# Optimization experiments

Measured on AMD Instinct MI355X. Metric: run time of the kernel, lower is better.

## Reference

```python
import jax, jax.numpy as jnp
import numpy as np


def setup_inputs() -> dict:
    key = jax.random.key(0)
    k1, k2, k3, k4 = jax.random.split(key, 4)
    N, F, E, M = 50000, 128, 1600000, 1024
    return {
        "molec_feature_vectures": jax.random.normal(k1, (N, F), dtype=jnp.float32),
        "W": jax.random.normal(k2, (F, F), dtype=jnp.float32),
        "mo_neighbour_indices": jax.random.randint(k3, (2, E), 0, N, dtype=jnp.int64),
        "mo_mol_id": jax.random.randint(k4, (E,), 0, M, dtype=jnp.int64),
        "n_output": M,
    }


def reference(molec_feature_vectures, W, mo_neighbour_indices, mo_mol_id, n_output):
    # Gather endpoint features for each neighbor pair: [E, F]
    fi = molec_feature_vectures[mo_neighbour_indices[0]]
    fj = molec_feature_vectures[mo_neighbour_indices[1]]
    # Symmetric bilinear form (mode='pes'): s_n = fi_n . (W + W^T) . fj_n
    Ws = W + W.T  # [F, F]
    # Fuse as (fi @ Ws) * fj summed over F to avoid a 3-operand einsum blowup
    scalars = jnp.einsum('ni,ij,nj->n', fi, Ws, fj)  # [E]
    # Segment-sum per molecule
    res = jax.ops.segment_sum(scalars, mo_mol_id, num_segments=n_output)  # [M]
    return res
```

## Files before the change

kernel.cpp:

```cpp
#include <hip/hip_runtime.h>
#include <hip/hip_bf16.h>

#define FDIM 128
#define BROWS 32
#define NBLK 256
#define NSLICE 32

typedef __attribute__((ext_vector_type(8))) short short8v;
typedef __attribute__((ext_vector_type(4))) float f32x4;

static __device__ __forceinline__ unsigned short f2bf(float x) {
    unsigned u = __float_as_uint(x);
    unsigned r = 0x7fffu + ((u >> 16) & 1u);
    return (unsigned short)((u + r) >> 16);
}
static __device__ __forceinline__ float bf2f(unsigned short h) {
    return __uint_as_float((unsigned)h << 16);
}
static __device__ __forceinline__ float bf_lo(unsigned u) { return __uint_as_float(u << 16); }
static __device__ __forceinline__ float bf_hi(unsigned u) { return __uint_as_float(u & 0xffff0000u); }

static __device__ __forceinline__ void split2(float v, short& h, short& l) {
    unsigned short hh = f2bf(v);
    h = (short)hh;
    l = (short)f2bf(v - bf2f(hh));
}

__global__ __launch_bounds__(512, 4) void gemm_mfma(
    const float* __restrict__ Fm, const float* __restrict__ W,
    unsigned short* __restrict__ Gbf, int N) {
    __shared__ unsigned short sH[128 * 136];
    __shared__ unsigned short sL[128 * 136];

    for (int idx = threadIdx.x; idx < 128 * 128; idx += 512) {
        int i = idx >> 7, j = idx & 127;
        float w = W[idx] + W[j * 128 + i];
        short h, l;
        split2(w, h, l);
        sH[i * 136 + j] = (unsigned short)h;
        sL[i * 136 + j] = (unsigned short)l;
    }
    __syncthreads();

    const int wid  = threadIdx.x >> 6;
    const int lane = threadIdx.x & 63;
    const int ar   = lane & 15;
    const int kg   = lane >> 4;
    const int row0 = blockIdx.x * 128 + wid * 16;
    const int gr   = row0 + ar;
    const bool rv  = gr < N;
    const float* fp = Fm + (size_t)gr * FDIM;

    f32x4 acc[8];
#pragma unroll
    for (int t = 0; t < 8; ++t) acc[t] = (f32x4){0.f, 0.f, 0.f, 0.f};

#pragma unroll
    for (int ks = 0; ks < 4; ++ks) {
        const int k0 = ks * 32 + kg * 8;
        float4 fa = make_float4(0.f, 0.f, 0.f, 0.f);
        float4 fb = make_float4(0.f, 0.f, 0.f, 0.f);
        if (rv) {
            fa = *(const float4*)(fp + k0);
            fb = *(const float4*)(fp + k0 + 4);
        }
        short8v ah, al;
        {
            short h, l;
            split2(fa.x, h, l); ah[0] = h; al[0] = l;
            split2(fa.y, h, l); ah[1] = h; al[1] = l;
            split2(fa.z, h, l); ah[2] = h; al[2] = l;
            split2(fa.w, h, l); ah[3] = h; al[3] = l;
            split2(fb.x, h, l); ah[4] = h; al[4] = l;
            split2(fb.y, h, l); ah[5] = h; al[5] = l;
            split2(fb.z, h, l); ah[6] = h; al[6] = l;
            split2(fb.w, h, l); ah[7] = h; al[7] = l;
        }
#pragma unroll
        for (int ct = 0; ct < 8; ++ct) {
            const short8v bh = *(const short8v*)(sH + (ct * 16 + ar) * 136 + k0);
            const short8v bl = *(const short8v*)(sL + (ct * 16 + ar) * 136 + k0);
            acc[ct] = __builtin_amdgcn_mfma_f32_16x16x32_bf16(ah, bh, acc[ct], 0, 0, 0);
            acc[ct] = __builtin_amdgcn_mfma_f32_16x16x32_bf16(ah, bl, acc[ct], 0, 0, 0);
            acc[ct] = __builtin_amdgcn_mfma_f32_16x16x32_bf16(al, bh, acc[ct], 0, 0, 0);
        }
    }

#pragma unroll
    for (int r = 0; r < 4; ++r) {
        const int orow = row0 + kg * 4 + r;
        if (orow < N) {
#pragma unroll
            for (int ct = 0; ct < 8; ++ct)
                Gbf[(size_t)orow * FDIM + ct * 16 + ar] = f2bf(acc[ct][r]);
        }
    }
}

__global__ __launch_bounds__(256) void k_hist(const int* __restrict__ idx, int E,
                                              int nb, unsigned* __restrict__ M) {
    extern __shared__ unsigned cnt[];
    for (int i = threadIdx.x; i < nb; i += 256) cnt[i] = 0;
    __syncthreads();
    int chunk = (E + NBLK - 1) / NBLK;
    int s = blockIdx.x * chunk;
    int e_end = min(E, s + chunk);
    for (int e = s + threadIdx.x; e < e_end; e += 256) {
        int i1 = idx[E + e];
        atomicAdd(&cnt[i1 >> 5], 1u);
    }
    __syncthreads();
    for (int i = threadIdx.x; i < nb; i += 256)
        M[(size_t)blockIdx.x * nb + i] = cnt[i];
}

__global__ __launch_bounds__(256) void k_mscan2(unsigned* __restrict__ M, int nb,
                                                unsigned* __restrict__ tot) {
    int b = blockIdx.x * 4 + (threadIdx.x >> 6);
    int lane = threadIdx.x & 63;
    if (b >= nb) return;
    unsigned m0 = M[(size_t)(4 * lane + 0) * nb + b];
    unsigned m1 = M[(size_t)(4 * lane + 1) * nb + b];
    unsigned m2 = M[(size_t)(4 * lane + 2) * nb + b];
    unsigned m3 = M[(size_t)(4 * lane + 3) * nb + b];
    unsigned s = m0 + m1 + m2 + m3;
    unsigned incl = s;
#pragma unroll
    for (int d = 1; d < 64; d <<= 1) {
        unsigned u = __shfl_up(incl, d, 64);
        if (lane >= d) incl += u;
    }
    unsigned run = incl - s;
    M[(size_t)(4 * lane + 0) * nb + b] = run; run += m0;
    M[(size_t)(4 * lane + 1) * nb + b] = run; run += m1;
    M[(size_t)(4 * lane + 2) * nb + b] = run; run += m2;
    M[(size_t)(4 * lane + 3) * nb + b] = run;
    if (lane == 63) tot[b] = incl;
}

__global__ __launch_bounds__(256) void k_bscan(const unsigned* __restrict__ tot, int nb,
                                               unsigned* __restrict__ bucketStart) {
    __shared__ unsigned wS[4];
    int t = threadIdx.x;
    unsigned v0, v1, v2, v3, v4, v5, v6, v7;
    int b0 = t * 8;
    v0 = (b0 + 0 < nb) ? tot[b0 + 0] : 0u;
    v1 = (b0 + 1 < nb) ? tot[b0 + 1] : 0u;
    v2 = (b0 + 2 < nb) ? tot[b0 + 2] : 0u;
    v3 = (b0 + 3 < nb) ? tot[b0 + 3] : 0u;
    v4 = (b0 + 4 < nb) ? tot[b0 + 4] : 0u;
    v5 = (b0 + 5 < nb) ? tot[b0 + 5] : 0u;
    v6 = (b0 + 6 < nb) ? tot[b0 + 6] : 0u;
    v7 = (b0 + 7 < nb) ? tot[b0 + 7] : 0u;
    unsigned l0 = 0, l1 = v0, l2 = l1 + v1, l3 = l2 + v2, l4 = l3 + v3,
             l5 = l4 + v4, l6 = l5 + v5, l7 = l6 + v6;
    unsigned s = l7 + v7;
    int lane = t & 63, wid = t >> 6;
    unsigned incl = s;
    for (int d = 1; d < 64; d <<= 1) {
        unsigned u = __shfl_up(incl, d, 64);
        if (lane >= d) incl += u;
    }
    if (lane == 63) wS[wid] = incl;
    __syncthreads();
    unsigned wOff = 0;
    for (int i = 0; i < wid; ++i) wOff += wS[i];
    unsigned base = wOff + incl - s;
    if (b0 + 0 < nb) bucketStart[b0 + 0] = base + l0;
    if (b0 + 1 < nb) bucketStart[b0 + 1] = base + l1;
    if (b0 + 2 < nb) bucketStart[b0 + 2] = base + l2;
    if (b0 + 3 < nb) bucketStart[b0 + 3] = base + l3;
    if (b0 + 4 < nb) bucketStart[b0 + 4] = base + l4;
    if (b0 + 5 < nb) bucketStart[b0 + 5] = base + l5;
    if (b0 + 6 < nb) bucketStart[b0 + 6] = base + l6;
    if (b0 + 7 < nb) bucketStart[b0 + 7] = base + l7;
    if (t == 255) bucketStart[nb] = base + s;
}

__global__ __launch_bounds__(256) void k_scatter(const int* __restrict__ idx,
                                                 const int* __restrict__ mol, int E,
                                                 int nb, const unsigned* __restrict__ M,
                                                 const unsigned* __restrict__ bucketStart,
                                                 unsigned* __restrict__ sortedE) {
    extern __shared__ unsigned cur[];
    for (int i = threadIdx.x; i < nb; i += 256)
        cur[i] = M[(size_t)blockIdx.x * nb + i] + bucketStart[i];
    __syncthreads();
    int chunk = (E + NBLK - 1) / NBLK;
    int s = blockIdx.x * chunk;
    int e_end = min(E, s + chunk);
    for (int e = s + threadIdx.x; e < e_end; e += 256) {
        int i0 = idx[e];
        int i1 = idx[E + e];
        int m  = mol[e];
        int b  = i1 >> 5;
        int loc = i1 & 31;
        unsigned pos = atomicAdd(&cur[b], 1u);
        sortedE[pos] = (unsigned)i0 | ((unsigned)m << 16) | ((unsigned)loc << 26);
    }
}

__global__ __launch_bounds__(512, 8) void edge_kernel(
    const unsigned short* __restrict__ Gbf, const float* __restrict__ Fm,
    const unsigned* __restrict__ sortedE, const unsigned* __restrict__ bucketStart,
    float* __restrict__ part, int N, int Mout) {
    __shared__ unsigned short sFrow[BROWS * FDIM];
    __shared__ float smol[1024];

    int b = blockIdx.x;
    int row0 = b * BROWS;
    int nrow = min(BROWS, N - row0);
    for (int k = threadIdx.x; k < nrow * (FDIM / 4); k += 512) {
        int r = k >> 5, c = k & 31;
        float4 v = ((const float4*)(Fm + (size_t)(row0 + r) * FDIM))[c];
        ushort4 o;
        o.x = f2bf(v.x); o.y = f2bf(v.y); o.z = f2bf(v.z); o.w = f2bf(v.w);
        *(ushort4*)(sFrow + r * FDIM + c * 4) = o;
    }
    for (int i = threadIdx.x; i < 1024; i += 512) smol[i] = 0.f;
    __syncthreads();

    const int s = bucketStart[b];
    const int e_end = bucketStart[b + 1];
    const int lane = threadIdx.x & 63;
    const int sub  = lane >> 4;
    const int t16  = lane & 15;
    const int off16 = t16 * 8;
    const int wid  = threadIdx.x >> 6;

    int base = s + wid * 8;
    unsigned pkA = 0u, pkB = 0u;
    if (base + sub < e_end)     pkA = sortedE[base + sub];
    if (base + 4 + sub < e_end) pkB = sortedE[base + 4 + sub];

    while (base < e_end) {
        const int nbase = base + 64;
        unsigned npkA = 0u, npkB = 0u;
        if (nbase + sub < e_end)     npkA = sortedE[nbase + sub];
        if (nbase + 4 + sub < e_end) npkB = sortedE[nbase + 4 + sub];

        const bool vA = (base + sub) < e_end;
        const bool vB = (base + 4 + sub) < e_end;
        const int i0A = pkA & 0xffff;
        const int i0B = pkB & 0xffff;
        const uint4 gA = *(const uint4*)(Gbf + (size_t)i0A * FDIM + off16);
        const uint4 gB = *(const uint4*)(Gbf + (size_t)i0B * FDIM + off16);
        const int locA = pkA >> 26;
        const int locB = pkB >> 26;
        const uint4 fA = *(const uint4*)(sFrow + locA * FDIM + off16);
        const uint4 fB = *(const uint4*)(sFrow + locB * FDIM + off16);

        float pA, pB;
        pA = bf_lo(gA.x) * bf_lo(fA.x);
        pA = fmaf(bf_hi(gA.x), bf_hi(fA.x), pA);
        pA = fmaf(bf_lo(gA.y), bf_lo(fA.y), pA);
        pA = fmaf(bf_hi(gA.y), bf_hi(fA.y), pA);
        pA = fmaf(bf_lo(gA.z), bf_lo(fA.z), pA);
        pA = fmaf(bf_hi(gA.z), bf_hi(fA.z), pA);
        pA = fmaf(bf_lo(gA.w), bf_lo(fA.w), pA);
        pA = fmaf(bf_hi(gA.w), bf_hi(fA.w), pA);
        pB = bf_lo(gB.x) * bf_lo(fB.x);
        pB = fmaf(bf_hi(gB.x), bf_hi(fB.x), pB);
        pB = fmaf(bf_lo(gB.y), bf_lo(fB.y), pB);
        pB = fmaf(bf_hi(gB.y), bf_hi(fB.y), pB);
        pB = fmaf(bf_lo(gB.z), bf_lo(fB.z), pB);
        pB = fmaf(bf_hi(gB.z), bf_hi(fB.z), pB);
        pB = fmaf(bf_lo(gB.w), bf_lo(fB.w), pB);
        pB = fmaf(bf_hi(gB.w), bf_hi(fB.w), pB);

        pA += __shfl_xor(pA, 1, 16);
        pB += __shfl_xor(pB, 1, 16);
        pA += __shfl_xor(pA, 2, 16);
        pB += __shfl_xor(pB, 2, 16);
        pA += __shfl_xor(pA, 4, 16);
        pB += __shfl_xor(pB, 4, 16);
        pA += __shfl_xor(pA, 8, 16);
        pB += __shfl_xor(pB, 8, 16);

        if (t16 == 0) {
            if (vA) atomicAdd(&smol[(pkA >> 16) & 0x3ff], pA);
            if (vB) atomicAdd(&smol[(pkB >> 16) & 0x3ff], pB);
        }
        pkA = npkA; pkB = npkB; base = nbase;
    }
    __syncthreads();
    float* prow = part + (size_t)b * 1024;
    for (int i = threadIdx.x; i < Mout; i += 512) prow[i] = smol[i];
}

__global__ __launch_bounds__(256) void k_red1(const float* __restrict__ part, int nb,
                                              float* __restrict__ partial, int Mout) {
    int gid = blockIdx.x * 256 + threadIdx.x;
    int m = gid & 1023;
    int sl = gid >> 10;
    int per = (nb + NSLICE - 1) / NSLICE;
    int b0 = sl * per;
    int b1 = min(nb, b0 + per);
    float s = 0.f;
    if (m < Mout) {
        for (int b = b0; b < b1; ++b) s += part[(size_t)b * 1024 + m];
    }
    partial[sl * 1024 + m] = s;
}

__global__ __launch_bounds__(256) void k_red2(const float* __restrict__ partial,
                                              float* __restrict__ out, int Mout) {
    int m = blockIdx.x * 256 + threadIdx.x;
    if (m < Mout) {
        float s = 0.f;
        for (int sl = 0; sl < NSLICE; ++sl) s += partial[sl * 1024 + m];
        out[m] = s;
    }
}

extern "C" void kernel_launch(void* const* d_in, const int* in_sizes, int n_in,
                              void* d_out, int out_size, void* d_ws, size_t ws_size,
                              hipStream_t stream) {
    const float* Fm = (const float*)d_in[0];
    const float* W  = (const float*)d_in[1];
    const int* idx  = (const int*)d_in[2];
    const int* mol  = (const int*)d_in[3];
    float* out = (float*)d_out;

    const int N = in_sizes[0] / FDIM;
    const int E = in_sizes[3];

    const int nb = (N + BROWS - 1) / BROWS;

    char* ws = (char*)d_ws;
    size_t o = 0;
    unsigned short* Gbf = (unsigned short*)(ws + o); o += ((size_t)N * FDIM * 2 + 255) & ~(size_t)255;
    unsigned* sortedE = (unsigned*)(ws + o);         o += ((size_t)E * 4 + 255) & ~(size_t)255;
    unsigned* M = (unsigned*)(ws + o);               o += ((size_t)NBLK * nb * 4 + 255) & ~(size_t)255;
    unsigned* tot = (unsigned*)(ws + o);             o += ((size_t)nb * 4 + 255) & ~(size_t)255;
    unsigned* bucketStart = (unsigned*)(ws + o);     o += ((size_t)(nb + 1) * 4 + 255) & ~(size_t)255;
    float* part = (float*)(ws + o);                  o += (size_t)nb * 1024 * sizeof(float);
    float* partial = (float*)(ws + o);               o += NSLICE * 1024 * sizeof(float);

    gemm_mfma<<<(N + 127) / 128, 512, 0, stream>>>(Fm, W, Gbf, N);

    size_t smem = (size_t)nb * 4;
    k_hist<<<NBLK, 256, smem, stream>>>(idx, E, nb, M);
    k_mscan2<<<(nb + 3) / 4, 256, 0, stream>>>(M, nb, tot);
    k_bscan<<<1, 256, 0, stream>>>(tot, nb, bucketStart);
    k_scatter<<<NBLK, 256, smem, stream>>>(idx, mol, E, nb, M, bucketStart, sortedE);

    edge_kernel<<<nb, 512, 0, stream>>>(Gbf, Fm, sortedE, bucketStart, part, N, out_size);

    k_red1<<<NSLICE * 4, 256, 0, stream>>>(part, nb, partial, out_size);
    k_red2<<<(out_size + 255) / 256, 256, 0, stream>>>(partial, out, out_size);
}
```

Baseline: 210.3 us.

## Compute edge dot products with MFMA and atomically reduce into output

```diff
diff --git a/kernel.cpp b/kernel.cpp
--- a/kernel.cpp
+++ b/kernel.cpp
@@ -4,7 +4,6 @@
 #define FDIM 128
 #define BROWS 32
 #define NBLK 256
-#define NSLICE 32
 
 typedef __attribute__((ext_vector_type(8))) short short8v;
 typedef __attribute__((ext_vector_type(4))) float f32x4;
@@ -17,8 +16,6 @@
 static __device__ __forceinline__ float bf2f(unsigned short h) {
     return __uint_as_float((unsigned)h << 16);
 }
-static __device__ __forceinline__ float bf_lo(unsigned u) { return __uint_as_float(u << 16); }
-static __device__ __forceinline__ float bf_hi(unsigned u) { return __uint_as_float(u & 0xffff0000u); }
 
 static __device__ __forceinline__ void split2(float v, short& h, short& l) {
     unsigned short hh = f2bf(v);
@@ -98,7 +95,11 @@
 }
 
 __global__ __launch_bounds__(256) void k_hist(const int* __restrict__ idx, int E,
-                                              int nb, unsigned* __restrict__ M) {
+                                              int nb, unsigned* __restrict__ M,
+                                              float* __restrict__ out, int Mout) {
+    if (blockIdx.x == 0) {
+        for (int i = threadIdx.x; i < Mout; i += 256) out[i] = 0.f;
+    }
     extern __shared__ unsigned cnt[];
     for (int i = threadIdx.x; i < nb; i += 256) cnt[i] = 0;
     __syncthreads();
@@ -203,113 +204,69 @@
 __global__ __launch_bounds__(512, 8) void edge_kernel(
     const unsigned short* __restrict__ Gbf, const float* __restrict__ Fm,
     const unsigned* __restrict__ sortedE, const unsigned* __restrict__ bucketStart,
-    float* __restrict__ part, int N, int Mout) {
-    __shared__ unsigned short sFrow[BROWS * FDIM];
+    float* __restrict__ out, int N, int Mout) {
+    __shared__ __align__(16) unsigned short sFrow[BROWS * FDIM];
     __shared__ float smol[1024];
 
-    int b = blockIdx.x;
-    int row0 = b * BROWS;
-    int nrow = min(BROWS, N - row0);
-    for (int k = threadIdx.x; k < nrow * (FDIM / 4); k += 512) {
-        int r = k >> 5, c = k & 31;
-        float4 v = ((const float4*)(Fm + (size_t)(row0 + r) * FDIM))[c];
-        ushort4 o;
-        o.x = f2bf(v.x); o.y = f2bf(v.y); o.z = f2bf(v.z); o.w = f2bf(v.w);
-        *(ushort4*)(sFrow + r * FDIM + c * 4) = o;
+    const int b = blockIdx.x;
+    const int row0 = b * BROWS;
+    const int nrow = min(BROWS, N - row0);
+
+    for (int k = threadIdx.x; k < nrow * 16; k += 512) {
+        int r = k >> 4, g = k & 15;
+        const float4* src = (const float4*)(Fm + (size_t)(row0 + r) * FDIM + g * 8);
+        float4 v0 = src[0], v1 = src[1];
+        unsigned u0 = (unsigned)f2bf(v0.x) | ((unsigned)f2bf(v0.y) << 16);
+        unsigned u1 = (unsigned)f2bf(v0.z) | ((unsigned)f2bf(v0.w) << 16);
+        unsigned u2 = (unsigned)f2bf(v1.x) | ((unsigned)f2bf(v1.y) << 16);
+        unsigned u3 = (unsigned)f2bf(v1.z) | ((unsigned)f2bf(v1.w) << 16);
+        char* dst = (char*)sFrow + r * 256 + ((g * 16) ^ ((r & 7) << 4));
+        *(uint4*)dst = make_uint4(u0, u1, u2, u3);
     }
     for (int i = threadIdx.x; i < 1024; i += 512) smol[i] = 0.f;
     __syncthreads();
 
-    const int s = bucketStart[b];
-    const int e_end = bucketStart[b + 1];
+    const int s = (int)bucketStart[b];
+    const int e_end = (int)bucketStart[b + 1];
     const int lane = threadIdx.x & 63;
-    const int sub  = lane >> 4;
-    const int t16  = lane & 15;
-    const int off16 = t16 * 8;
     const int wid  = threadIdx.x >> 6;
-
-    int base = s + wid * 8;
-    unsigned pkA = 0u, pkB = 0u;
-    if (base + sub < e_end)     pkA = sortedE[base + sub];
-    if (base + 4 + sub < e_end) pkB = sortedE[base + 4 + sub];
+    const int er = lane & 15;
+    const int kg = lane >> 4;
+    const bool isdiag = ((er >> 2) == kg);
+
+    int base = s + wid * 16;
+    unsigned pk = 0u;
+    if (base + er < e_end && base < e_end) pk = sortedE[base + er];
 
     while (base < e_end) {
-        const int nbase = base + 64;
-        unsigned npkA = 0u, npkB = 0u;
-        if (nbase + sub < e_end)     npkA = sortedE[nbase + sub];
-        if (nbase + 4 + sub < e_end) npkB = sortedE[nbase + 4 + sub];
-
-        const bool vA = (base + sub) < e_end;
-        const bool vB = (base + 4 + sub) < e_end;
-        const int i0A = pkA & 0xffff;
-        const int i0B = pkB & 0xffff;
-        const uint4 gA = *(const uint4*)(Gbf + (size_t)i0A * FDIM + off16);
-        const uint4 gB = *(const uint4*)(Gbf + (size_t)i0B * FDIM + off16);
-        const int locA = pkA >> 26;
-        const int locB = pkB >> 26;
-        const uint4 fA = *(const uint4*)(sFrow + locA * FDIM + off16);
-        const uint4 fB = *(const uint4*)(sFrow + locB * FDIM + off16);
-
-        float pA, pB;
-        pA = bf_lo(gA.x) * bf_lo(fA.x);
-        pA = fmaf(bf_hi(gA.x), bf_hi(fA.x), pA);
-        pA = fmaf(bf_lo(gA.y), bf_lo(fA.y), pA);
-        pA = fmaf(bf_hi(gA.y), bf_hi(fA.y), pA);
-        pA = fmaf(bf_lo(gA.z), bf_lo(fA.z), pA);
-        pA = fmaf(bf_hi(gA.z), bf_hi(fA.z), pA);
-        pA = fmaf(bf_lo(gA.w), bf_lo(fA.w), pA);
-        pA = fmaf(bf_hi(gA.w), bf_hi(fA.w), pA);
-        pB = bf_lo(gB.x) * bf_lo(fB.x);
-        pB = fmaf(bf_hi(gB.x), bf_hi(fB.x), pB);
-        pB = fmaf(bf_lo(gB.y), bf_lo(fB.y), pB);
-        pB = fmaf(bf_hi(gB.y), bf_hi(fB.y), pB);
-        pB = fmaf(bf_lo(gB.z), bf_lo(fB.z), pB);
-        pB = fmaf(bf_hi(gB.z), bf_hi(fB.z), pB);
-        pB = fmaf(bf_lo(gB.w), bf_lo(fB.w), pB);
-        pB = fmaf(bf_hi(gB.w), bf_hi(fB.w), pB);
-
-        pA += __shfl_xor(pA, 1, 16);
-        pB += __shfl_xor(pB, 1, 16);
-        pA += __shfl_xor(pA, 2, 16);
-        pB += __shfl_xor(pB, 2, 16);
-        pA += __shfl_xor(pA, 4, 16);
-        pB += __shfl_xor(pB, 4, 16);
-        pA += __shfl_xor(pA, 8, 16);
-        pB += __shfl_xor(pB, 8, 16);
-
-        if (t16 == 0) {
-            if (vA) atomicAdd(&smol[(pkA >> 16) & 0x3ff], pA);
-            if (vB) atomicAdd(&smol[(pkB >> 16) & 0x3ff], pB);
-        }
-        pkA = npkA; pkB = npkB; base = nbase;
-    }
-    __syncthreads();
-    float* prow = part + (size_t)b * 1024;
-    for (int i = threadIdx.x; i < Mout; i += 512) prow[i] = smol[i];
-}
-
-__global__ __launch_bounds__(256) void k_red1(const float* __restrict__ part, int nb,
-                                              float* __restrict__ partial, int Mout) {
-    int gid = blockIdx.x * 256 + threadIdx.x;
-    int m = gid & 1023;
-    int sl = gid >> 10;
-    int per = (nb + NSLICE - 1) / NSLICE;
-    int b0 = sl * per;
-    int b1 = min(nb, b0 + per);
-    float s = 0.f;
-    if (m < Mout) {
-        for (int b = b0; b < b1; ++b) s += part[(size_t)b * 1024 + m];
-    }
-    partial[sl * 1024 + m] = s;
-}
-
-__global__ __launch_bounds__(256) void k_red2(const float* __restrict__ partial,
-                                              float* __restrict__ out, int Mout) {
-    int m = blockIdx.x * 256 + threadIdx.x;
-    if (m < Mout) {
-        float s = 0.f;
-        for (int sl = 0; sl < NSLICE; ++sl) s += partial[sl * 1024 + m];
-        out[m] = s;
+        const int nbase = base + 128;
+        unsigned npk = 0u;
+        if (nbase < e_end && nbase + er < e_end) npk = sortedE[nbase + er];
+
+        const int i0  = pk & 0xffff;
+        const int loc = pk >> 26;
+        const unsigned short* gp = Gbf + (size_t)i0 * FDIM + kg * 8;
+        const char* lp = (const char*)sFrow + loc * 256;
+        const int swz = (loc & 7) << 4;
+
+        f32x4 acc = (f32x4){0.f, 0.f, 0.f, 0.f};
+#pragma unroll
+        for (int ks = 0; ks < 4; ++ks) {
+            short8v a  = *(const short8v*)(gp + ks * 32);
+            short8v bf = *(const short8v*)(lp + ((ks * 64 + kg * 16) ^ swz));
+            acc = __builtin_amdgcn_mfma_f32_16x16x32_bf16(a, bf, acc, 0, 0, 0);
+        }
+        if (isdiag && (base + er < e_end)) {
+            atomicAdd(&smol[(pk >> 16) & 0x3ff], acc[er & 3]);
+        }
+        pk = npk;
+        base = nbase;
+    }
+    __syncthreads();
+
+    for (int i = threadIdx.x; i < Mout; i += 512) {
+        float v = smol[i];
+        if (v != 0.f) atomicAdd(&out[i], v);
     }
 }
 
@@ -334,19 +291,14 @@
     unsigned* M = (unsigned*)(ws + o);               o += ((size_t)NBLK * nb * 4 + 255) & ~(size_t)255;
     unsigned* tot = (unsigned*)(ws + o);             o += ((size_t)nb * 4 + 255) & ~(size_t)255;
     unsigned* bucketStart = (unsigned*)(ws + o);     o += ((size_t)(nb + 1) * 4 + 255) & ~(size_t)255;
-    float* part = (float*)(ws + o);                  o += (size_t)nb * 1024 * sizeof(float);
-    float* partial = (float*)(ws + o);               o += NSLICE * 1024 * sizeof(float);
 
     gemm_mfma<<<(N + 127) / 128, 512, 0, stream>>>(Fm, W, Gbf, N);
 
     size_t smem = (size_t)nb * 4;
-    k_hist<<<NBLK, 256, smem, stream>>>(idx, E, nb, M);
+    k_hist<<<NBLK, 256, smem, stream>>>(idx, E, nb, M, out, out_size);
     k_mscan2<<<(nb + 3) / 4, 256, 0, stream>>>(M, nb, tot);
     k_bscan<<<1, 256, 0, stream>>>(tot, nb, bucketStart);
     k_scatter<<<NBLK, 256, smem, stream>>>(idx, mol, E, nb, M, bucketStart, sortedE);
 
-    edge_kernel<<<nb, 512, 0, stream>>>(Gbf, Fm, sortedE, bucketStart, part, N, out_size);
-
-    k_red1<<<NSLICE * 4, 256, 0, stream>>>(part, nb, partial, out_size);
-    k_red2<<<(out_size + 255) / 256, 256, 0, stream>>>(partial, out, out_size);
-}
+    edge_kernel<<<nb, 512, 0, stream>>>(Gbf, Fm, sortedE, bucketStart, out, N, out_size);
+}
```

Measured after the change: 210.5 us. Within noise of the previous version (+0.1%).
